# Kernel tuning notes

Hardware: AMD Instinct MI355X
Metric: run time of the kernel (lower is better)

The kernel has to match this reference:

```python
import jax, jax.numpy as jnp
import numpy as np
from math import factorial

N_NODES = 10000
N_EDGES = 320000
FEAT = 32
NBASIS = 8
RMAX = 6.0
ZMAX = 119


def _cg(j1, m1, j2, m2, j3, m3):
    if m1 + m2 != m3 or j3 < abs(j1 - j2) or j3 > j1 + j2:
        return 0.0
    f = lambda n: float(factorial(n))
    pre = ((2 * j3 + 1) * f(j1 + j2 - j3) * f(j1 - j2 + j3) * f(-j1 + j2 + j3) / f(j1 + j2 + j3 + 1)) ** 0.5
    pre *= (f(j3 + m3) * f(j3 - m3) * f(j1 - m1) * f(j1 + m1) * f(j2 - m2) * f(j2 + m2)) ** 0.5
    s = 0.0
    for k in range(j1 + j2 + j3 + 1):
        d = [k, j1 + j2 - j3 - k, j1 - m1 - k, j2 + m2 - k, j3 - j2 + m1 + k, j3 - j1 - m2 + k]
        if min(d) < 0:
            continue
        s += (-1) ** k / (f(d[0]) * f(d[1]) * f(d[2]) * f(d[3]) * f(d[4]) * f(d[5]))
    return pre * s


def _u_real(l):
    # complex->real spherical harmonics unitary transform
    U = np.zeros((2 * l + 1, 2 * l + 1), dtype=complex)
    s2 = 1.0 / np.sqrt(2.0)
    for m in range(-l, l + 1):
        i = m + l
        if m == 0:
            U[i, l] = 1.0
        elif m > 0:
            U[i, l + m] = ((-1) ** m) * s2
            U[i, l - m] = s2
        else:
            U[i, l + m] = 1j * s2
            U[i, l - m] = -1j * ((-1) ** m) * s2
    return U


def _real_cg():
    # real Clebsch-Gordan coupling coefficients for l<=2, shape (9,9,9), sparse
    off = [0, 1, 4]
    C = np.zeros((9, 9, 9))
    Us = [_u_real(l) for l in range(3)]
    for l1 in range(3):
        for l2 in range(3):
            for l3 in range(3):
                if l3 < abs(l1 - l2) or l3 > l1 + l2:
                    continue
                cg = np.zeros((2 * l1 + 1, 2 * l2 + 1, 2 * l3 + 1))
                for m1 in range(-l1, l1 + 1):
                    for m2 in range(-l2, l2 + 1):
                        m3 = m1 + m2
                        if abs(m3) <= l3:
                            cg[m1 + l1, m2 + l2, m3 + l3] = _cg(l1, m1, l2, m2, l3, m3)
                blk = np.einsum('ia,jb,kc,abc->ijk', Us[l1], Us[l2], np.conj(Us[l3]), cg.astype(complex))
                C[off[l1]:off[l1] + 2 * l1 + 1, off[l2]:off[l2] + 2 * l2 + 1, off[l3]:off[l3] + 2 * l3 + 1] = blk.real + blk.imag
    return C

CGC = jnp.asarray(_real_cg(), dtype=jnp.float32)
SL = [slice(0, 1), slice(1, 4), slice(4, 9)]
PATHS0 = [(0, 0, 0), (0, 1, 1), (0, 2, 2)]
PATHS1 = [(l1, l2, l3) for l1 in range(3) for l2 in range(3) for l3 in range(3) if abs(l1 - l2) <= l3 <= l1 + l2]
PATHS2 = [(0, 0, 0), (1, 1, 0), (2, 2, 0)]


def _real_sph(u):
    x, y, z = u[:, 0], u[:, 1], u[:, 2]
    c0 = 0.28209479177387814
    c1 = 0.4886025119029199
    c2a = 1.0925484305920792
    c2b = 0.31539156525252005
    c2c = 0.5462742152960396
    return jnp.stack([c0 * jnp.ones_like(x), c1 * y, c1 * z, c1 * x,
                      c2a * x * y, c2a * y * z, c2b * (3.0 * z * z - 1.0), c2a * x * z,
                      c2c * (x * x - y * y)], axis=-1)


def _message_pass(x, rad, Y, src, dst, W, paths, out_dim, n_nodes):
    # gather src node features -> per-edge CG tensor product with (radial x Ylm) basis -> scatter-add to dst
    xs = x[src, 0]  # (E, Dx, F)
    msg = jnp.zeros((rad.shape[0], out_dim, x.shape[-1]), x.dtype)
    for p, (l1, l2, l3) in enumerate(paths):
        w = rad @ W[p]  # (E, F) learned radial path weights
        contrib = jnp.einsum('abc,eaf,eb,ef->ecf', CGC[SL[l1], SL[l2], SL[l3]], xs[:, SL[l1], :], Y[:, SL[l2]], w)
        msg = msg.at[:, SL[l3], :].add(contrib)
    y = jax.ops.segment_sum(msg, dst, num_segments=n_nodes)
    return y[:, None]  # (N, 1, out_dim, F)


def _eadd(a, b):
    if a.shape[2] == b.shape[2]:
        return a + b
    if a.shape[2] < b.shape[2]:
        a, b = b, a
    return a.at[:, :, :b.shape[2], :].add(b)


def _edense(x, K, b):
    # equivariant Dense: shared kernel across degrees, bias only on scalar (l=0) channel
    y = jnp.einsum('npdf,fg->npdg', x, K)
    return y.at[:, :, 0, :].add(b)


def _esilu(x):
    # silu on scalars, sigmoid(scalar)-gated scaling on l>0 components (equivariant)
    if x.shape[2] == 1:
        return jax.nn.silu(x)
    s = x[:, :, 0:1, :]
    return jnp.concatenate([jax.nn.silu(s), x[:, :, 1:, :] * jax.nn.sigmoid(s)], axis=2)


def _forward(dr_vec, Z, neighbor_idxs, embed, wmp0, wmp1, wmp2, dk1, db1, dk2, db2):
    idx_i, idx_j = neighbor_idxs[0], neighbor_idxs[1]
    nN = Z.shape[0]
    r = jnp.sqrt(jnp.sum(dr_vec * dr_vec, axis=-1) + 1e-12)  # (E,)
    u = dr_vec / r[:, None]
    n = jnp.arange(1, NBASIS + 1, dtype=dr_vec.dtype)
    rad = jnp.sqrt(2.0 / RMAX) * jnp.sin(n * jnp.pi * r[:, None] / RMAX) / r[:, None]  # Bessel radial basis
    t = jnp.clip(r / RMAX, 0.0, 1.0 - 1e-6)
    cut = jnp.where(r < RMAX, jnp.exp(1.0 - 1.0 / (1.0 - t * t)), 0.0)  # smooth cutoff
    mask = (idx_i != idx_j).astype(dr_vec.dtype)  # mask padding/self edges
    rad = rad * (cut * mask)[:, None]
    Y = _real_sph(u)  # (E, 9)
    x = embed[Z][:, None, None, :]  # (N, 1, 1, F)
    for it, (paths, W) in enumerate([(PATHS0, wmp0), (PATHS1, wmp1), (PATHS2, wmp2)]):
        last = it == 2
        y = _message_pass(x, rad, Y, idx_j, idx_i, W, paths, 1 if last else 9, nN)
        if last:
            x = x[:, :, 0:1, :]  # change_max_degree_or_type -> scalars only
        y = _eadd(x, y)
        y = _edense(y, dk1[it], db1[it])
        y = _esilu(y)
        y = _edense(y, dk2[it], db2[it])
        x = _eadd(x, y)
    return x[:, 0, 0, :]


def setup_inputs():
    key = jax.random.key(0)
    ks = jax.random.split(key, 10)
    dr_vec = 2.0 * jax.random.normal(ks[0], (N_EDGES, 3), jnp.float32)
    Z = jax.random.randint(ks[1], (N_NODES,), 0, ZMAX)
    neighbor_idxs = jax.random.randint(ks[2], (2, N_EDGES), 0, N_NODES)
    embed = jax.random.normal(ks[3], (ZMAX, FEAT), jnp.float32)
    sB = 1.0 / np.sqrt(NBASIS)
    wmp0 = sB * jax.random.normal(ks[4], (len(PATHS0), NBASIS, FEAT), jnp.float32)
    wmp1 = sB * jax.random.normal(ks[5], (len(PATHS1), NBASIS, FEAT), jnp.float32)
    wmp2 = sB * jax.random.normal(ks[6], (len(PATHS2), NBASIS, FEAT), jnp.float32)
    sF = 1.0 / np.sqrt(FEAT)
    dense_k1 = sF * jax.random.normal(ks[7], (3, FEAT, FEAT), jnp.float32)
    dense_b1 = jnp.zeros((3, FEAT), jnp.float32)
    dense_k2 = 0.1 * sF * jax.random.normal(ks[8], (3, FEAT, FEAT), jnp.float32)
    dense_b2 = jnp.zeros((3, FEAT), jnp.float32)
    return {"dr_vec": dr_vec, "Z": Z, "neighbor_idxs": neighbor_idxs, "embed": embed,
            "wmp0": wmp0, "wmp1": wmp1, "wmp2": wmp2,
            "dense_k1": dense_k1, "dense_b1": dense_b1, "dense_k2": dense_k2, "dense_b2": dense_b2}


def reference(dr_vec, Z, neighbor_idxs, embed, wmp0, wmp1, wmp2, dense_k1, dense_b1, dense_k2, dense_b2):
    return _forward(dr_vec, Z, neighbor_idxs, embed, wmp0, wmp1, wmp2, dense_k1, dense_b1, dense_k2, dense_b2)
```

## Files before the change

kernel.cpp:

```cpp
#include <hip/hip_runtime.h>
#include <type_traits>
#include <cstdint>
#include <cstddef>

#define N_FEAT 32
#define NBASIS 8
#define SPAN   16
#define BSLOTS 8
#define BEDGES (SPAN*BSLOTS)

namespace cgc {

constexpr double dfact(int n){ double r=1.0; for(int i=2;i<=n;++i) r*=(double)i; return r; }

constexpr double dsqrt(double x){
  if(x<=0.0) return 0.0;
  double g = x>1.0 ? x : 1.0;
  for(int i=0;i<200;++i){ double ng = 0.5*(g + x/g); if(ng==g) break; g=ng; }
  return g;
}

constexpr double cg1(int j1,int m1,int j2,int m2,int j3,int m3){
  int adiff = j1-j2; if(adiff<0) adiff=-adiff;
  if(m1+m2!=m3 || j3<adiff || j3>j1+j2) return 0.0;
  double pre = dsqrt((double)(2*j3+1)*dfact(j1+j2-j3)*dfact(j1-j2+j3)*dfact(-j1+j2+j3)/dfact(j1+j2+j3+1));
  pre = pre*dsqrt(dfact(j3+m3)*dfact(j3-m3)*dfact(j1-m1)*dfact(j1+m1)*dfact(j2-m2)*dfact(j2+m2));
  double s=0.0;
  for(int k=0;k<=j1+j2+j3;++k){
    int d1=j1+j2-j3-k, d2=j1-m1-k, d3=j2+m2-k, d4=j3-j2+m1+k, d5=j3-j1-m2+k;
    if(d1<0||d2<0||d3<0||d4<0||d5<0) continue;
    double term = 1.0/(dfact(k)*dfact(d1)*dfact(d2)*dfact(d3)*dfact(d4)*dfact(d5));
    s += (k&1)? -term : term;
  }
  return pre*s;
}

struct Tab { float v[9][9][9]; };

constexpr Tab make(){
  Tab T{};
  int off[3]={0,1,4};
  double Ure[3][5][5]={}, Uim[3][5][5]={};
  const double s2 = dsqrt(0.5);
  for(int l=0;l<3;++l){
    for(int m=-l;m<=l;++m){
      int i=m+l;
      if(m==0){ Ure[l][i][l]=1.0; }
      else if(m>0){
        Ure[l][i][l+m] = ((m&1)? -1.0:1.0)*s2;
        Ure[l][i][l-m] = s2;
      } else {
        int am=-m;
        Uim[l][i][l+m] = s2;
        Uim[l][i][l-m] = -(((am&1)?-1.0:1.0))*s2;
      }
    }
  }
  for(int l1=0;l1<3;++l1) for(int l2=0;l2<3;++l2) for(int l3=0;l3<3;++l3){
    int lo = l1-l2; if(lo<0) lo=-lo;
    if(l3<lo || l3>l1+l2) continue;
    int d1=2*l1+1, d2=2*l2+1, d3=2*l3+1;
    double cg[5][5][5]={};
    for(int m1=-l1;m1<=l1;++m1) for(int m2=-l2;m2<=l2;++m2){
      int m3=m1+m2;
      if(m3>=-l3 && m3<=l3) cg[m1+l1][m2+l2][m3+l3] = cg1(l1,m1,l2,m2,l3,m3);
    }
    double t1re[5][5][5]={}, t1im[5][5][5]={};
    for(int a=0;a<d1;++a) for(int b=0;b<d2;++b) for(int k=0;k<d3;++k){
      double sre=0, sim=0;
      for(int c=0;c<d3;++c){
        double g=cg[a][b][c]; if(g==0.0) continue;
        sre += g*Ure[l3][k][c];
        sim -= g*Uim[l3][k][c];
      }
      t1re[a][b][k]=sre; t1im[a][b][k]=sim;
    }
    double t2re[5][5][5]={}, t2im[5][5][5]={};
    for(int a=0;a<d1;++a) for(int j=0;j<d2;++j) for(int k=0;k<d3;++k){
      double sre=0,sim=0;
      for(int b=0;b<d2;++b){
        double ur=Ure[l2][j][b], ui=Uim[l2][j][b];
        if(ur==0.0&&ui==0.0) continue;
        sre += ur*t1re[a][b][k]-ui*t1im[a][b][k];
        sim += ur*t1im[a][b][k]+ui*t1re[a][b][k];
      }
      t2re[a][j][k]=sre; t2im[a][j][k]=sim;
    }
    for(int i=0;i<d1;++i) for(int j=0;j<d2;++j) for(int k=0;k<d3;++k){
      double sre=0,sim=0;
      for(int a=0;a<d1;++a){
        double ur=Ure[l1][i][a], ui=Uim[l1][i][a];
        if(ur==0.0&&ui==0.0) continue;
        sre += ur*t2re[a][j][k]-ui*t2im[a][j][k];
        sim += ur*t2im[a][j][k]+ui*t2re[a][j][k];
      }
      T.v[off[l1]+i][off[l2]+j][off[l3]+k] = (float)(sre+sim);
    }
  }
  return T;
}

constexpr Tab T = make();

}

template<int I, int N, typename F>
__device__ __forceinline__ void sfor(F&& f){
  if constexpr (I < N){
    f(std::integral_constant<int,I>{});
    sfor<I+1,N>(static_cast<F&&>(f));
  }
}

constexpr int LOFF[3] = {0,1,4};

struct PS0 {
  static constexpr int NP=3;
  static constexpr int L[3][3]={{0,0,0},{0,1,1},{0,2,2}};
  static constexpr int ALO=0, AHI=1, OD=9, WOFF=0;
  static constexpr int MINW=4;
};
struct PS1a {
  static constexpr int NP=9;
  static constexpr int L[9][3]={{0,0,0},{0,1,1},{0,2,2},
                                {1,0,1},{1,1,0},{1,1,1},{1,1,2},{1,2,1},{1,2,2}};
  static constexpr int ALO=0, AHI=4, OD=9, WOFF=0;
  static constexpr int MINW=3;
};
struct PS1b {
  static constexpr int NP=6;
  static constexpr int L[6][3]={{2,0,2},{2,1,1},{2,1,2},{2,2,0},{2,2,1},{2,2,2}};
  static constexpr int ALO=4, AHI=9, OD=9, WOFF=9*NBASIS*N_FEAT;
  static constexpr int MINW=3;
};
struct PS2 {
  static constexpr int NP=3;
  static constexpr int L[3][3]={{0,0,0},{1,1,0},{2,2,0}};
  static constexpr int ALO=0, AHI=9, OD=1, WOFF=0;
  static constexpr int MINW=3;
};

__global__ void zero_kernel(int* __restrict__ a, int n){
  int i = blockIdx.x*256 + threadIdx.x;
  if(i<n) a[i]=0;
}

__global__ void count_kernel(const int* __restrict__ dst, int* __restrict__ cnt, int E){
  int e = blockIdx.x*256 + threadIdx.x;
  if(e<E) atomicAdd(&cnt[dst[e]], 1);
}

__global__ void __launch_bounds__(1024) scan_kernel(const int* __restrict__ cnt,
                                                    int* __restrict__ row_ptr,
                                                    int* __restrict__ cursor, int n){
  __shared__ int part[1024];
  const int tid = threadIdx.x;
  const int chunk = (n + 1023) >> 10;
  const int s0 = tid*chunk;
  const int s1 = (s0+chunk < n) ? s0+chunk : n;
  int s=0;
  for(int i=s0;i<s1;++i) s += cnt[i];
  part[tid]=s; __syncthreads();
  for(int off=1; off<1024; off<<=1){
    int v = 0;
    if(tid>=off) v = part[tid-off];
    __syncthreads();
    part[tid] += v;
    __syncthreads();
  }
  int run = part[tid] - s;
  for(int i=s0;i<s1;++i){
    int cv = cnt[i];
    row_ptr[i]=run; cursor[i]=run;
    run += cv;
  }
  if(tid==1023) row_ptr[n] = part[1023];
}

__global__ void fill_kernel(const int* __restrict__ dst, const int* __restrict__ src,
                            int* __restrict__ cursor, int* __restrict__ perm,
                            int* __restrict__ srcs, int* __restrict__ dsts, int E){
  int e = blockIdx.x*256 + threadIdx.x;
  if(e<E){
    int d = dst[e];
    int pos = atomicAdd(&cursor[d], 1);
    perm[e] = pos;
    srcs[pos] = src[e];
    dsts[pos] = d;
  }
}

__global__ void geom_kernel(const float* __restrict__ dr, const int* __restrict__ ii,
                            const int* __restrict__ jj, const int* __restrict__ perm,
                            float* __restrict__ radY, int E){
  int e = blockIdx.x*256 + threadIdx.x;
  if(e>=E) return;
  float dx=dr[3*e], dy=dr[3*e+1], dz=dr[3*e+2];
  float r2 = fmaf(dx,dx,fmaf(dy,dy,fmaf(dz,dz,1e-12f)));
  float r = sqrtf(r2);
  float inv = 1.f/r;
  float ux=dx*inv, uy=dy*inv, uz=dz*inv;
  float t = r*(1.f/6.f);
  t = fminf(fmaxf(t,0.f), 1.f-1e-6f);
  float cut = 0.f;
  if (r < 6.f) cut = expf(1.f - 1.f/(1.f - t*t));
  if (ii[e]==jj[e]) cut = 0.f;
  float base = 0.57735026918962576f * inv * cut;
  float* o = radY + (size_t)perm[e]*20;
  const float pir = 0.52359877559829887f * r;
  #pragma unroll
  for(int nb=1; nb<=8; ++nb) o[nb-1] = base * sinf((float)nb * pir);
  o[8]  = 0.28209479177387814f;
  o[9]  = 0.4886025119029199f*uy;
  o[10] = 0.4886025119029199f*uz;
  o[11] = 0.4886025119029199f*ux;
  o[12] = 1.0925484305920792f*ux*uy;
  o[13] = 1.0925484305920792f*uy*uz;
  o[14] = 0.31539156525252005f*(3.f*uz*uz-1.f);
  o[15] = 1.0925484305920792f*ux*uz;
  o[16] = 0.5462742152960396f*(ux*ux-uy*uy);
  o[17]=0.f; o[18]=0.f; o[19]=0.f;
}

__global__ void init_kernel(const float* __restrict__ embed, const int* __restrict__ Z,
                            float* __restrict__ xA, int nN){
  int i = blockIdx.x*256 + threadIdx.x;
  if(i >= nN*N_FEAT) return;
  int n = i>>5, f = i&31;
  xA[(size_t)n*288 + f] = embed[Z[n]*N_FEAT + f];
}

template<class PS>
__global__ void __launch_bounds__(256, PS::MINW) mp_kernel(
    const int* __restrict__ dsts, const int* __restrict__ srcs,
    const float* __restrict__ radY, const float* __restrict__ x_in,
    const float* __restrict__ W, float* __restrict__ ymsg, int E)
{
  constexpr int NP = PS::NP;
  constexpr int ALO = PS::ALO, AHI = PS::AHI, DA = AHI-ALO;
  constexpr int OD = PS::OD;

  __shared__ float sRad[BEDGES*20];
  __shared__ int   sSrc[BEDGES];
  __shared__ int   sDst[BEDGES];

  const int tid  = threadIdx.x;
  const int base = blockIdx.x * BEDGES;
  const int nE   = (base + BEDGES <= E) ? BEDGES : (E - base);

  {
    const float4* g4 = (const float4*)(radY + (size_t)base*20);
    float4* s4 = (float4*)sRad;
    const int n4 = nE*5;
    for (int i=tid; i<n4; i+=256) s4[i] = g4[i];
    for (int i=tid; i<nE;  i+=256){ sSrc[i]=srcs[base+i]; sDst[i]=dsts[base+i]; }
  }
  __syncthreads();

  const int f  = tid & 31;
  int k        = (tid>>5)*SPAN;
  const int k1 = (k+SPAN < nE) ? k+SPAN : nE;
  if (k >= nE) return;

  float Wreg[NP][NBASIS];
  sfor<0,NP>([&](auto P){
    sfor<0,NBASIS>([&](auto Q){
      Wreg[P.value][Q.value] = W[PS::WOFF + (P.value*NBASIS+Q.value)*N_FEAT + f];
    });
  });

  float msg[OD];
  sfor<0,OD>([&](auto C){ msg[C.value]=0.f; });

  int d = sDst[k];
  float xsA[DA];
  {
    const float* xb = x_in + (size_t)sSrc[k]*288 + ALO*N_FEAT + f;
    sfor<0,DA>([&](auto A){ xsA[A.value] = xb[A.value*N_FEAT]; });
  }

  for (;;){
    const int kn = k + 1;
    const bool more = kn < k1;
    float xsB[DA]; int dn = -1;
    if (more){
      const float* xb = x_in + (size_t)sSrc[kn]*288 + ALO*N_FEAT + f;
      sfor<0,DA>([&](auto A){ xsB[A.value] = xb[A.value*N_FEAT]; });
      dn = sDst[kn];
    }

    const float* rp = sRad + k*20;
    const float4 q0 = *(const float4*)(rp);
    const float4 q1 = *(const float4*)(rp+4);
    const float4 q2 = *(const float4*)(rp+8);
    const float4 q3 = *(const float4*)(rp+12);
    const float y8 = rp[16];
    const float rad[8] = {q0.x,q0.y,q0.z,q0.w,q1.x,q1.y,q1.z,q1.w};
    const float Yv[9]  = {q2.x,q2.y,q2.z,q2.w,q3.x,q3.y,q3.z,q3.w,y8};

    sfor<0,NP>([&](auto P){
      constexpr int p  = P.value;
      constexpr int l1 = PS::L[p][0], l2 = PS::L[p][1], l3 = PS::L[p][2];
      constexpr int o1 = LOFF[l1], o2 = LOFF[l2], o3 = LOFF[l3];
      float w = 0.f;
      sfor<0,NBASIS>([&](auto Q){ w = fmaf(rad[Q.value], Wreg[p][Q.value], w); });
      sfor<0,2*l2+1>([&](auto B){
        constexpr int b = B.value;
        const float yw = Yv[o2+b]*w;
        sfor<0,2*l1+1>([&](auto A){
          constexpr int a = A.value;
          sfor<0,2*l3+1>([&](auto C){
            constexpr int c = C.value;
            constexpr float cgv = cgc::T.v[o1+a][o2+b][o3+c];
            if constexpr (cgv > 1e-7f || cgv < -1e-7f){
              msg[o3+c] = fmaf(cgv*xsA[o1+a-ALO], yw, msg[o3+c]);
            }
          });
        });
      });
    });

    if (dn != d){
      float* yb = ymsg + ((size_t)d*OD)*N_FEAT + f;
      sfor<0,OD>([&](auto C){
        atomicAdd(yb + C.value*N_FEAT, msg[C.value]);
        msg[C.value] = 0.f;
      });
      d = dn;
    }
    if (!more) break;

    sfor<0,DA>([&](auto A){ xsA[A.value] = xsB[A.value]; });
    k = kn;
  }
}

template<int DX>
__global__ void __launch_bounds__(256) nodeA_kernel(
    const float* __restrict__ xin, const float* __restrict__ ymsg,
    const float* __restrict__ K1, const float* __restrict__ b1,
    const float* __restrict__ K2, const float* __restrict__ b2,
    float* __restrict__ xout, int nN)
{
  __shared__ float sK1[1024], sK2[1024], sb1[32], sb2[32];
  __shared__ float tb[8][9][32];
  const int tid = threadIdx.x;
  for(int i=tid;i<1024;i+=256){ sK1[i]=K1[i]; sK2[i]=K2[i]; }
  if(tid<32){ sb1[tid]=b1[tid]; sb2[tid]=b2[tid]; }
  __syncthreads();
  const int h = tid>>5, f = tid&31;
  const int n = blockIdx.x*8 + h;
  const bool valid = n < nN;
  const int nc = valid ? n : 0;
  float xi[9];
  #pragma unroll
  for(int c=0;c<9;++c){
    float t = ymsg[((size_t)nc*9+c)*32+f];
    float x = 0.f;
    if (c<DX) x = xin[((size_t)nc*9+c)*32+f];
    xi[c]=x;
    tb[h][c][f] = t + x;
  }
  __syncthreads();
  float u[9];
  #pragma unroll
  for(int c=0;c<9;++c){
    float acc = (c==0) ? sb1[f] : 0.f;
    #pragma unroll
    for(int g=0;g<32;++g) acc = fmaf(tb[h][c][g], sK1[g*32+f], acc);
    u[c]=acc;
  }
  const float gate = 1.f/(1.f+expf(-u[0]));
  __syncthreads();
  #pragma unroll
  for(int c=0;c<9;++c) tb[h][c][f] = u[c]*gate;
  __syncthreads();
  #pragma unroll
  for(int c=0;c<9;++c){
    float acc = (c==0) ? sb2[f] : 0.f;
    #pragma unroll
    for(int g=0;g<32;++g) acc = fmaf(tb[h][c][g], sK2[g*32+f], acc);
    if (valid) xout[((size_t)n*9+c)*32+f] = acc + ((c<DX) ? xi[c] : 0.f);
  }
}

__global__ void __launch_bounds__(256) nodeB_kernel(
    const float* __restrict__ xin, const float* __restrict__ msg0,
    const float* __restrict__ K1, const float* __restrict__ b1,
    const float* __restrict__ K2, const float* __restrict__ b2,
    float* __restrict__ out, int nN)
{
  __shared__ float sK1[1024], sK2[1024], sb1[32], sb2[32];
  __shared__ float tb[8][32];
  const int tid = threadIdx.x;
  for(int i=tid;i<1024;i+=256){ sK1[i]=K1[i]; sK2[i]=K2[i]; }
  if(tid<32){ sb1[tid]=b1[tid]; sb2[tid]=b2[tid]; }
  __syncthreads();
  const int h = tid>>5, f = tid&31;
  const int n = blockIdx.x*8 + h;
  const bool valid = n < nN;
  const int nc = valid ? n : 0;
  const float x0 = xin[(size_t)nc*288 + f];
  tb[h][f] = msg0[(size_t)nc*32+f] + x0;
  __syncthreads();
  float acc = sb1[f];
  #pragma unroll
  for(int g=0;g<32;++g) acc = fmaf(tb[h][g], sK1[g*32+f], acc);
  const float gate = 1.f/(1.f+expf(-acc));
  const float v = acc*gate;
  __syncthreads();
  tb[h][f] = v;
  __syncthreads();
  float acc2 = sb2[f];
  #pragma unroll
  for(int g=0;g<32;++g) acc2 = fmaf(tb[h][g], sK2[g*32+f], acc2);
  if (valid) out[(size_t)n*32+f] = x0 + acc2;
}

extern "C" void kernel_launch(void* const* d_in, const int* in_sizes, int n_in,
                              void* d_out, int out_size, void* d_ws, size_t ws_size,
                              hipStream_t stream) {
  const float* dr    = (const float*)d_in[0];
  const int*   Z     = (const int*)  d_in[1];
  const int*   nbr   = (const int*)  d_in[2];
  const float* embed = (const float*)d_in[3];
  const float* wmp0  = (const float*)d_in[4];
  const float* wmp1  = (const float*)d_in[5];
  const float* wmp2  = (const float*)d_in[6];
  const float* dk1   = (const float*)d_in[7];
  const float* db1   = (const float*)d_in[8];
  const float* dk2   = (const float*)d_in[9];
  const float* db2   = (const float*)d_in[10];
  const int nN = in_sizes[1];
  const int E  = in_sizes[2]/2;
  const int* idx_i = nbr;
  const int* idx_j = nbr + E;

  uintptr_t base = (uintptr_t)d_ws;
  auto alloc = [&](size_t bytes)->void*{
    uintptr_t p = (base + 255) & ~(uintptr_t)255;
    base = p + bytes;
    return (void*)p;
  };
  float* radY    = (float*)alloc((size_t)E*20*4);
  int*   cnt     = (int*)  alloc((size_t)nN*4);
  int*   cursor  = (int*)  alloc((size_t)nN*4);
  int*   row_ptr = (int*)  alloc((size_t)(nN+1)*4);
  int*   perm    = (int*)  alloc((size_t)E*4);
  int*   srcs    = (int*)  alloc((size_t)E*4);
  int*   dsts    = (int*)  alloc((size_t)E*4);
  float* xA      = (float*)alloc((size_t)nN*288*4);
  float* xB      = (float*)alloc((size_t)nN*288*4);
  float* ymsg    = (float*)alloc((size_t)nN*288*4);

  const int gE = (E+255)/256;
  const int gN = (nN+255)/256;

  zero_kernel <<<gN, 256, 0, stream>>>(cnt, nN);
  count_kernel<<<gE, 256, 0, stream>>>(idx_i, cnt, E);
  scan_kernel <<<1, 1024, 0, stream>>>(cnt, row_ptr, cursor, nN);
  fill_kernel <<<gE, 256, 0, stream>>>(idx_i, idx_j, cursor, perm, srcs, dsts, E);

  geom_kernel <<<gE, 256, 0, stream>>>(dr, idx_i, idx_j, perm, radY, E);
  init_kernel <<<(nN*N_FEAT+255)/256, 256, 0, stream>>>(embed, Z, xA, nN);

  const int gND = (nN+7)/8;
  const int gMP = (E + BEDGES - 1) / BEDGES;
  const size_t ymsgBytes = (size_t)nN*288*4;

  hipMemsetAsync(ymsg, 0, ymsgBytes, stream);
  mp_kernel<PS0><<<gMP, 256, 0, stream>>>(dsts, srcs, radY, xA, wmp0, ymsg, E);
  nodeA_kernel<1><<<gND, 256, 0, stream>>>(xA, ymsg, dk1, db1, dk2, db2, xB, nN);
  hipMemsetAsync(ymsg, 0, ymsgBytes, stream);
  mp_kernel<PS1a><<<gMP, 256, 0, stream>>>(dsts, srcs, radY, xB, wmp1, ymsg, E);
  mp_kernel<PS1b><<<gMP, 256, 0, stream>>>(dsts, srcs, radY, xB, wmp1, ymsg, E);
  nodeA_kernel<9><<<gND, 256, 0, stream>>>(xB, ymsg, dk1+1024, db1+32, dk2+1024, db2+32, xA, nN);
  hipMemsetAsync(ymsg, 0, (size_t)nN*32*4, stream);
  mp_kernel<PS2><<<gMP, 256, 0, stream>>>(dsts, srcs, radY, xA, wmp2, ymsg, E);
  nodeB_kernel<<<gND, 256, 0, stream>>>(xA, ymsg, dk1+2048, db1+64, dk2+2048, db2+64,
                                        (float*)d_out, nN);
}
```

Baseline: 433.1 us.

## Switch message passing to per-node CSR segments without atomics

Message passing now assigns one warp to each destination node: it walks that node's CSR row range, stages edge data in shared memory in chunks, and writes the result with plain stores (or read-modify-write for the second path pass). This removes the float atomics, the ymsg memsets and the dsts array, and adds a two-deep register prefetch of source features. The cost is load imbalance, since warps with high-degree nodes hold up their block. Every warp also waits at block-wide barriers for each chunk it stages, even when few of the edges belong to it.

```diff
diff --git a/kernel.cpp b/kernel.cpp
--- a/kernel.cpp
+++ b/kernel.cpp
@@ -5,9 +5,8 @@
 
 #define N_FEAT 32
 #define NBASIS 8
-#define SPAN   16
-#define BSLOTS 8
-#define BEDGES (SPAN*BSLOTS)
+#define NSLOT  8
+#define CAPE   288
 
 namespace cgc {
 
@@ -179,14 +178,13 @@
 
 __global__ void fill_kernel(const int* __restrict__ dst, const int* __restrict__ src,
                             int* __restrict__ cursor, int* __restrict__ perm,
-                            int* __restrict__ srcs, int* __restrict__ dsts, int E){
+                            int* __restrict__ srcs, int E){
   int e = blockIdx.x*256 + threadIdx.x;
   if(e<E){
     int d = dst[e];
     int pos = atomicAdd(&cursor[d], 1);
     perm[e] = pos;
     srcs[pos] = src[e];
-    dsts[pos] = d;
   }
 }
 
@@ -230,37 +228,30 @@
   xA[(size_t)n*288 + f] = embed[Z[n]*N_FEAT + f];
 }
 
-template<class PS>
+template<class PS, bool ACCUM>
 __global__ void __launch_bounds__(256, PS::MINW) mp_kernel(
-    const int* __restrict__ dsts, const int* __restrict__ srcs,
+    const int* __restrict__ row_ptr, const int* __restrict__ srcs,
     const float* __restrict__ radY, const float* __restrict__ x_in,
-    const float* __restrict__ W, float* __restrict__ ymsg, int E)
+    const float* __restrict__ W, float* __restrict__ ymsg, int nN)
 {
   constexpr int NP = PS::NP;
   constexpr int ALO = PS::ALO, AHI = PS::AHI, DA = AHI-ALO;
   constexpr int OD = PS::OD;
 
-  __shared__ float sRad[BEDGES*20];
-  __shared__ int   sSrc[BEDGES];
-  __shared__ int   sDst[BEDGES];
-
-  const int tid  = threadIdx.x;
-  const int base = blockIdx.x * BEDGES;
-  const int nE   = (base + BEDGES <= E) ? BEDGES : (E - base);
-
-  {
-    const float4* g4 = (const float4*)(radY + (size_t)base*20);
-    float4* s4 = (float4*)sRad;
-    const int n4 = nE*5;
-    for (int i=tid; i<n4; i+=256) s4[i] = g4[i];
-    for (int i=tid; i<nE;  i+=256){ sSrc[i]=srcs[base+i]; sDst[i]=dsts[base+i]; }
-  }
-  __syncthreads();
-
-  const int f  = tid & 31;
-  int k        = (tid>>5)*SPAN;
-  const int k1 = (k+SPAN < nE) ? k+SPAN : nE;
-  if (k >= nE) return;
+  __shared__ float sRad[CAPE*20];
+  __shared__ int   sSrc[CAPE];
+
+  const int tid = threadIdx.x;
+  const int h = tid>>5, f = tid&31;
+  const int n0 = blockIdx.x*NSLOT;
+  const int n  = n0 + h;
+  const int nHi = (n0+NSLOT < nN) ? n0+NSLOT : nN;
+  const bool valid = (n < nN);
+
+  const int bLo = row_ptr[n0];
+  const int bHi = row_ptr[nHi];
+  const int eLo = valid ? row_ptr[n]   : bHi;
+  const int eHi = valid ? row_ptr[n+1] : bHi;
 
   float Wreg[NP][NBASIS];
   sfor<0,NP>([&](auto P){
@@ -272,66 +263,85 @@
   float msg[OD];
   sfor<0,OD>([&](auto C){ msg[C.value]=0.f; });
 
-  int d = sDst[k];
-  float xsA[DA];
-  {
-    const float* xb = x_in + (size_t)sSrc[k]*288 + ALO*N_FEAT + f;
-    sfor<0,DA>([&](auto A){ xsA[A.value] = xb[A.value*N_FEAT]; });
-  }
-
-  for (;;){
-    const int kn = k + 1;
-    const bool more = kn < k1;
-    float xsB[DA]; int dn = -1;
-    if (more){
-      const float* xb = x_in + (size_t)sSrc[kn]*288 + ALO*N_FEAT + f;
-      sfor<0,DA>([&](auto A){ xsB[A.value] = xb[A.value*N_FEAT]; });
-      dn = sDst[kn];
-    }
-
-    const float* rp = sRad + k*20;
-    const float4 q0 = *(const float4*)(rp);
-    const float4 q1 = *(const float4*)(rp+4);
-    const float4 q2 = *(const float4*)(rp+8);
-    const float4 q3 = *(const float4*)(rp+12);
-    const float y8 = rp[16];
-    const float rad[8] = {q0.x,q0.y,q0.z,q0.w,q1.x,q1.y,q1.z,q1.w};
-    const float Yv[9]  = {q2.x,q2.y,q2.z,q2.w,q3.x,q3.y,q3.z,q3.w,y8};
-
-    sfor<0,NP>([&](auto P){
-      constexpr int p  = P.value;
-      constexpr int l1 = PS::L[p][0], l2 = PS::L[p][1], l3 = PS::L[p][2];
-      constexpr int o1 = LOFF[l1], o2 = LOFF[l2], o3 = LOFF[l3];
-      float w = 0.f;
-      sfor<0,NBASIS>([&](auto Q){ w = fmaf(rad[Q.value], Wreg[p][Q.value], w); });
-      sfor<0,2*l2+1>([&](auto B){
-        constexpr int b = B.value;
-        const float yw = Yv[o2+b]*w;
-        sfor<0,2*l1+1>([&](auto A){
-          constexpr int a = A.value;
-          sfor<0,2*l3+1>([&](auto C){
-            constexpr int c = C.value;
-            constexpr float cgv = cgc::T.v[o1+a][o2+b][o3+c];
-            if constexpr (cgv > 1e-7f || cgv < -1e-7f){
-              msg[o3+c] = fmaf(cgv*xsA[o1+a-ALO], yw, msg[o3+c]);
-            }
+  for (int base = bLo; base < bHi; base += CAPE){
+    const int nStage = (bHi - base < CAPE) ? (bHi - base) : CAPE;
+    __syncthreads();
+    {
+      const float4* g4 = (const float4*)(radY + (size_t)base*20);
+      float4* s4 = (float4*)sRad;
+      const int n4 = nStage*5;
+      for (int i=tid; i<n4; i+=256) s4[i] = g4[i];
+      for (int i=tid; i<nStage; i+=256) sSrc[i] = srcs[base+i];
+    }
+    __syncthreads();
+
+    const int lo = (eLo > base) ? eLo : base;
+    const int hiG = base + nStage;
+    const int hi = (eHi < hiG) ? eHi : hiG;
+    const int cnt = hi - lo;
+    if (cnt > 0){
+      const int k0 = lo - base;
+      const int kL = k0 + cnt - 1;
+      float xsA[DA], xsB[DA], xsC[DA];
+      {
+        const float* xb = x_in + (size_t)sSrc[k0]*288 + ALO*N_FEAT + f;
+        sfor<0,DA>([&](auto A){ xsA[A.value] = xb[A.value*N_FEAT]; });
+      }
+      {
+        const int kb = (k0+1 < kL) ? k0+1 : kL;
+        const float* xb = x_in + (size_t)sSrc[kb]*288 + ALO*N_FEAT + f;
+        sfor<0,DA>([&](auto A){ xsB[A.value] = xb[A.value*N_FEAT]; });
+      }
+      #pragma unroll 2
+      for (int i=0; i<cnt; ++i){
+        const int kc = k0 + i;
+        {
+          const int kp = (kc+2 < kL) ? kc+2 : kL;
+          const float* xb = x_in + (size_t)sSrc[kp]*288 + ALO*N_FEAT + f;
+          sfor<0,DA>([&](auto A){ xsC[A.value] = xb[A.value*N_FEAT]; });
+        }
+        const float* rp = sRad + kc*20;
+        const float4 q0 = *(const float4*)(rp);
+        const float4 q1 = *(const float4*)(rp+4);
+        const float4 q2 = *(const float4*)(rp+8);
+        const float4 q3 = *(const float4*)(rp+12);
+        const float y8 = rp[16];
+        const float rad[8] = {q0.x,q0.y,q0.z,q0.w,q1.x,q1.y,q1.z,q1.w};
+        const float Yv[9]  = {q2.x,q2.y,q2.z,q2.w,q3.x,q3.y,q3.z,q3.w,y8};
+
+        sfor<0,NP>([&](auto P){
+          constexpr int p  = P.value;
+          constexpr int l1 = PS::L[p][0], l2 = PS::L[p][1], l3 = PS::L[p][2];
+          constexpr int o1 = LOFF[l1], o2 = LOFF[l2], o3 = LOFF[l3];
+          float w = 0.f;
+          sfor<0,NBASIS>([&](auto Q){ w = fmaf(rad[Q.value], Wreg[p][Q.value], w); });
+          sfor<0,2*l2+1>([&](auto B){
+            constexpr int b = B.value;
+            const float yw = Yv[o2+b]*w;
+            sfor<0,2*l1+1>([&](auto A){
+              constexpr int a = A.value;
+              sfor<0,2*l3+1>([&](auto C){
+                constexpr int c = C.value;
+                constexpr float cgv = cgc::T.v[o1+a][o2+b][o3+c];
+                if constexpr (cgv > 1e-7f || cgv < -1e-7f){
+                  msg[o3+c] = fmaf(cgv*xsA[o1+a-ALO], yw, msg[o3+c]);
+                }
+              });
+            });
           });
         });
-      });
+
+        sfor<0,DA>([&](auto A){ xsA[A.value]=xsB[A.value]; xsB[A.value]=xsC[A.value]; });
+      }
+    }
+  }
+
+  if (valid){
+    float* yb = ymsg + (size_t)n*OD*N_FEAT + f;
+    sfor<0,OD>([&](auto C){
+      if constexpr (ACCUM) yb[C.value*N_FEAT] += msg[C.value];
+      else                 yb[C.value*N_FEAT]  = msg[C.value];
     });
-
-    if (dn != d){
-      float* yb = ymsg + ((size_t)d*OD)*N_FEAT + f;
-      sfor<0,OD>([&](auto C){
-        atomicAdd(yb + C.value*N_FEAT, msg[C.value]);
-        msg[C.value] = 0.f;
-      });
-      d = dn;
-    }
-    if (!more) break;
-
-    sfor<0,DA>([&](auto A){ xsA[A.value] = xsB[A.value]; });
-    k = kn;
   }
 }
 
@@ -448,7 +458,6 @@
   int*   row_ptr = (int*)  alloc((size_t)(nN+1)*4);
   int*   perm    = (int*)  alloc((size_t)E*4);
   int*   srcs    = (int*)  alloc((size_t)E*4);
-  int*   dsts    = (int*)  alloc((size_t)E*4);
   float* xA      = (float*)alloc((size_t)nN*288*4);
   float* xB      = (float*)alloc((size_t)nN*288*4);
   float* ymsg    = (float*)alloc((size_t)nN*288*4);
@@ -459,24 +468,20 @@
   zero_kernel <<<gN, 256, 0, stream>>>(cnt, nN);
   count_kernel<<<gE, 256, 0, stream>>>(idx_i, cnt, E);
   scan_kernel <<<1, 1024, 0, stream>>>(cnt, row_ptr, cursor, nN);
-  fill_kernel <<<gE, 256, 0, stream>>>(idx_i, idx_j, cursor, perm, srcs, dsts, E);
+  fill_kernel <<<gE, 256, 0, stream>>>(idx_i, idx_j, cursor, perm, srcs, E);
 
   geom_kernel <<<gE, 256, 0, stream>>>(dr, idx_i, idx_j, perm, radY, E);
   init_kernel <<<(nN*N_FEAT+255)/256, 256, 0, stream>>>(embed, Z, xA, nN);
 
   const int gND = (nN+7)/8;
-  const int gMP = (E + BEDGES - 1) / BEDGES;
-  const size_t ymsgBytes = (size_t)nN*288*4;
-
-  hipMemsetAsync(ymsg, 0, ymsgBytes, stream);
-  mp_kernel<PS0><<<gMP, 256, 0, stream>>>(dsts, srcs, radY, xA, wmp0, ymsg, E);
+  const int gMP = (nN+NSLOT-1)/NSLOT;
+
+  mp_kernel<PS0,false><<<gMP, 256, 0, stream>>>(row_ptr, srcs, radY, xA, wmp0, ymsg, nN);
   nodeA_kernel<1><<<gND, 256, 0, stream>>>(xA, ymsg, dk1, db1, dk2, db2, xB, nN);
-  hipMemsetAsync(ymsg, 0, ymsgBytes, stream);
-  mp_kernel<PS1a><<<gMP, 256, 0, stream>>>(dsts, srcs, radY, xB, wmp1, ymsg, E);
-  mp_kernel<PS1b><<<gMP, 256, 0, stream>>>(dsts, srcs, radY, xB, wmp1, ymsg, E);
+  mp_kernel<PS1a,false><<<gMP, 256, 0, stream>>>(row_ptr, srcs, radY, xB, wmp1, ymsg, nN);
+  mp_kernel<PS1b,true ><<<gMP, 256, 0, stream>>>(row_ptr, srcs, radY, xB, wmp1, ymsg, nN);
   nodeA_kernel<9><<<gND, 256, 0, stream>>>(xB, ymsg, dk1+1024, db1+32, dk2+1024, db2+32, xA, nN);
-  hipMemsetAsync(ymsg, 0, (size_t)nN*32*4, stream);
-  mp_kernel<PS2><<<gMP, 256, 0, stream>>>(dsts, srcs, radY, xA, wmp2, ymsg, E);
+  mp_kernel<PS2,false><<<gMP, 256, 0, stream>>>(row_ptr, srcs, radY, xA, wmp2, ymsg, nN);
   nodeB_kernel<<<gND, 256, 0, stream>>>(xA, ymsg, dk1+2048, db1+64, dk2+2048, db2+64,
                                         (float*)d_out, nN);
 }
```

Result: slower. 465.7 us (+7.5%).
